# Performance work log

Hardware: AMD Instinct MI355X
Metric: run time of the kernel (lower is better)

Reference implementation:

```python
import jax, jax.numpy as jnp
import numpy as np
import math

B, N, SEEDS, DIM, H = 16, 2048, 4, 512, 8
DS = DIM // H
EPS = 1e-5
LOG_2PI = math.log(2.0 * math.pi)


def setup_inputs() -> dict:
    key = jax.random.key(0)
    ks = jax.random.split(key, 12)
    s = 1.0 / math.sqrt(DIM)
    d = {}
    d["X"] = jax.random.normal(ks[0], (B, N, SEEDS, DIM), jnp.float32)
    # seed parameters (kaiming/xavier-ish init)
    d["M"] = jax.random.uniform(ks[1], (1, SEEDS, DIM), jnp.float32, -s, s) * math.sqrt(6.0)
    d["S"] = jax.random.uniform(ks[2], (1, SEEDS, DIM), jnp.float32, -s, s) * math.sqrt(6.0)
    d["p"] = jax.random.uniform(ks[3], (1, SEEDS), jnp.float32, -0.5, 0.5)
    # linear layers (PyTorch Linear: y = x @ W.T + b)
    d["Wk"] = jax.random.uniform(ks[4], (DIM, DIM), jnp.float32, -s, s)
    d["bk"] = jax.random.uniform(ks[5], (DIM,), jnp.float32, -s, s)
    d["Wv"] = jax.random.uniform(ks[6], (DIM, DIM), jnp.float32, -s, s)
    d["bv"] = jax.random.uniform(ks[7], (DIM,), jnp.float32, -s, s)
    d["Wo"] = jax.random.uniform(ks[8], (DIM, DIM), jnp.float32, -s, s)
    d["bo"] = jax.random.uniform(ks[9], (DIM,), jnp.float32, -s, s)
    # batchnorm affine params (init: weight=1, bias=0)
    d["g0"] = jnp.ones((SEEDS * DIM,), jnp.float32)
    d["b0"] = jnp.zeros((SEEDS * DIM,), jnp.float32)
    d["g1"] = jnp.ones((SEEDS * DIM,), jnp.float32)
    d["b1"] = jnp.zeros((SEEDS * DIM,), jnp.float32)
    return d


def _batchnorm(x, g, b):
    # BatchNorm1d in training mode: batch stats (biased variance), eps=1e-5
    m = x.mean(axis=0)
    v = x.var(axis=0)
    return g * (x - m) / jnp.sqrt(v + EPS) + b


def reference(X, M, S, p, Wk, bk, Wv, bv, Wo, bo, g0, b0, g1, b1):
    mu = M[0].reshape(SEEDS, H, DS)                      # [S,H,DS] per-head seeds
    sigma = jax.nn.softplus(S[0]).reshape(SEEDS, H, DS)  # [S,H,DS]
    logp = jnp.log(jax.nn.softmax(p[0], axis=-1))        # [S]

    K = (X @ Wk.T + bk).reshape(B, N, SEEDS, H, DS)
    V = (X @ Wv.T + bv).reshape(B, N, SEEDS, H, DS)

    # GMM log-likelihood scores: sum over per-head feature dim
    diff = K - mu                                        # [B,N,S,H,DS]
    ll = (-0.5 * LOG_2PI - jnp.log(sigma) - 0.5 * diff * diff / (sigma * sigma)).sum(-1)
    ll = ll + logp[:, None]                              # [B,N,S,H]

    A = jax.nn.softmax(ll / math.sqrt(DIM), axis=1)      # softmax over instances n
    O = mu + jnp.einsum('bnsh,bnshd->bshd', A, V)        # [B,S,H,DS]
    O = O.reshape(B, SEEDS, DIM)                         # head-major feature concat

    O = _batchnorm(O.reshape(B, SEEDS * DIM), g0, b0).reshape(B, SEEDS, DIM)
    O = O + jax.nn.relu(O @ Wo.T + bo)
    O = _batchnorm(O.reshape(B, SEEDS * DIM), g1, b1).reshape(B, SEEDS, DIM)
    return O
```

## Files before the change

### kernel.cpp

```cpp
#include <hip/hip_runtime.h>
#include <hip/hip_bf16.h>

typedef __attribute__((ext_vector_type(4))) float f32x4;
typedef __attribute__((ext_vector_type(8))) short bf16x8;

constexpr int NB = 16, NN = 2048, NS = 4, NDIM = 512, NH = 8, NDS = 64;
constexpr float LOG2PI = 1.8378770664093453f;
constexpr float INV_SQRT_DIM = 0.04419417382415922f;

__device__ inline short f2bf(float f) {
  __hip_bfloat16 h = __float2bfloat16(f);
  return *reinterpret_cast<short*>(&h);
}
__device__ inline float bf2f(short b) {
  union { unsigned u; float f; } v;
  v.u = ((unsigned)(unsigned short)b) << 16;
  return v.f;
}

__device__ inline void gld16(const void* g, void* l) {
  __builtin_amdgcn_global_load_lds(
      (const __attribute__((address_space(1))) void*)g,
      (__attribute__((address_space(3))) void*)l, 16, 0, 0);
}

__global__ __launch_bounds__(256) void prepcvt_kernel(
    const float* __restrict__ Wv, float* __restrict__ WvT,
    const float* __restrict__ Wk, short* __restrict__ Wkb,
    const float* __restrict__ Mp, const float* __restrict__ Sp,
    const float* __restrict__ pp, const float* __restrict__ bkp,
    float4* __restrict__ gmm, float* __restrict__ lp2,
    const float* __restrict__ X, short* __restrict__ Xb)
{
  const int blk = blockIdx.x;
  const int tid = threadIdx.x;
  if (blk < 1024) {
    const int idx = blk * 256 + tid;
    const int d = idx & 63;
    const int i = (idx >> 6) & 511;
    const int h = idx >> 15;
    WvT[idx] = Wv[(size_t)(h * 64 + d) * 512 + i];
  } else if (blk < 1152) {
    const int j = (blk - 1024) * 256 + tid;
    const float4 a = reinterpret_cast<const float4*>(Wk)[(size_t)j * 2];
    const float4 b = reinterpret_cast<const float4*>(Wk)[(size_t)j * 2 + 1];
    bf16x8 o;
    o[0] = f2bf(a.x); o[1] = f2bf(a.y); o[2] = f2bf(a.z); o[3] = f2bf(a.w);
    o[4] = f2bf(b.x); o[5] = f2bf(b.y); o[6] = f2bf(b.z); o[7] = f2bf(b.w);
    *reinterpret_cast<bf16x8*>(&Wkb[(size_t)j * 8]) = o;
  } else if (blk < 1160) {
    const int idx = (blk - 1152) * 256 + tid;
    const int Jg = idx & 511;
    const float sv = Sp[idx];
    const float sig = log1pf(expf(sv));
    float4 o;
    o.x = Mp[idx];
    o.y = (-0.5f * LOG2PI - logf(sig)) * INV_SQRT_DIM;
    o.z = (0.5f / (sig * sig)) * INV_SQRT_DIM;
    o.w = bkp[Jg];
    gmm[idx] = o;
    if (idx < 4) {
      const float p0 = pp[0], p1 = pp[1], p2 = pp[2], p3 = pp[3];
      const float pmx = fmaxf(fmaxf(p0, p1), fmaxf(p2, p3));
      const float lse = pmx + logf(expf(p0 - pmx) + expf(p1 - pmx) +
                                   expf(p2 - pmx) + expf(p3 - pmx));
      lp2[idx] = (pp[idx] - lse) * INV_SQRT_DIM;
    }
  } else {
    const int stride = 2048 * 256;
    for (int i = (blk - 1160) * 256 + tid; i < 8388608; i += stride) {
      const float4 a = reinterpret_cast<const float4*>(X)[(size_t)i * 2];
      const float4 b = reinterpret_cast<const float4*>(X)[(size_t)i * 2 + 1];
      bf16x8 o;
      o[0] = f2bf(a.x); o[1] = f2bf(a.y); o[2] = f2bf(a.z); o[3] = f2bf(a.w);
      o[4] = f2bf(b.x); o[5] = f2bf(b.y); o[6] = f2bf(b.z); o[7] = f2bf(b.w);
      *reinterpret_cast<bf16x8*>(&Xb[(size_t)i * 8]) = o;
    }
  }
}

__global__ __launch_bounds__(256) void kproj_kernel(
    const short* __restrict__ Xb, const short* __restrict__ Wkb,
    const float4* __restrict__ gmm, const float* __restrict__ lp2,
    float* __restrict__ ll_ws)
{
  __shared__ short As[2][128 * 64];
  __shared__ short Bs[2][128 * 64];

  const int bid0 = blockIdx.x;
  const int bid = (bid0 & 7) * 512 + (bid0 >> 3);
  const int ct = bid & 3;
  const int mt = bid >> 2;
  const int m0 = mt * 128;
  const int c0 = ct * 128;

  const int t = threadIdx.x;
  const int l = t & 63;
  const int w = t >> 6;
  const int wr = w >> 1, wc = w & 1;
  const int lg = l >> 4, lr = l & 15;

  f32x4 acc[4][4] = {};

  const int g8 = (l & 7) ^ (l >> 3);
  const size_t gxa = (size_t)(m0 + w * 32 + (l >> 3)) * NDIM + g8 * 8;
  const size_t gba = (size_t)(c0 + w * 32 + (l >> 3)) * NDIM + g8 * 8;
  const int dA = (w * 32) * 64;

  auto stage = [&](int buf, int ts) {
    const int k0 = ts << 6;
    #pragma unroll
    for (int q = 0; q < 4; ++q) {
      const size_t so = (size_t)(q * 8) * NDIM + k0;
      const int dd = dA + (q * 8) * 64;
      gld16(&Xb[gxa + so],  (char*)&As[buf][dd]);
      gld16(&Wkb[gba + so], (char*)&Bs[buf][dd]);
    }
  };

  auto compute = [&](int buf) {
    #pragma unroll
    for (int kk = 0; kk < 64; kk += 32) {
      bf16x8 a[4], b[4];
      #pragma unroll
      for (int i = 0; i < 4; ++i) {
        const int r = wr * 64 + i * 16 + lr;
        const int byte = r * 128 + ((((kk >> 3) + lg) ^ (lr & 7)) << 4);
        a[i] = *reinterpret_cast<const bf16x8*>((const char*)&As[buf][0] + byte);
      }
      #pragma unroll
      for (int j = 0; j < 4; ++j) {
        const int r = wc * 64 + j * 16 + lr;
        const int byte = r * 128 + ((((kk >> 3) + lg) ^ (lr & 7)) << 4);
        b[j] = *reinterpret_cast<const bf16x8*>((const char*)&Bs[buf][0] + byte);
      }
      #pragma unroll
      for (int i = 0; i < 4; ++i) {
        #pragma unroll
        for (int j = 0; j < 4; ++j)
          acc[i][j] = __builtin_amdgcn_mfma_f32_16x16x32_bf16(a[i], b[j], acc[i][j], 0, 0, 0);
      }
    }
  };

  stage(0, 0);
  __builtin_amdgcn_sched_barrier(0);
  for (int ts = 0; ts < 7; ++ts) {
    stage((ts + 1) & 1, ts + 1);
    asm volatile("s_waitcnt vmcnt(8)" ::: "memory");
    __builtin_amdgcn_s_barrier();
    compute(ts & 1);
    __builtin_amdgcn_s_barrier();
  }
  asm volatile("s_waitcnt vmcnt(0)" ::: "memory");
  __builtin_amdgcn_s_barrier();
  compute(1);
  __builtin_amdgcn_sched_barrier(0);


  const float l0 = lp2[0], l1 = lp2[1], l2 = lp2[2], l3 = lp2[3];
  const float lpv[4] = {l0, l1, l2, l3};

  float part[4][4];
  #pragma unroll
  for (int i = 0; i < 4; ++i)
    #pragma unroll
    for (int e = 0; e < 4; ++e) part[i][e] = 0.f;

  #pragma unroll
  for (int j = 0; j < 4; ++j) {
    const int Jg = c0 + wc * 64 + j * 16 + lr;
    #pragma unroll
    for (int e = 0; e < 4; ++e) {
      const float4 gw = gmm[e * NDIM + Jg];
      #pragma unroll
      for (int i = 0; i < 4; ++i) {
        const float kv = acc[i][j][e] + gw.w;
        const float d = kv - gw.x;
        part[i][e] += gw.y - d * d * gw.z;
      }
    }
  }
  #pragma unroll
  for (int off = 1; off < 16; off <<= 1) {
    #pragma unroll
    for (int i = 0; i < 4; ++i)
      #pragma unroll
      for (int e = 0; e < 4; ++e)
        part[i][e] += __shfl_xor(part[i][e], off, 64);
  }
  if (lr == 0) {
    const int h = ct * 2 + wc;
    #pragma unroll
    for (int i = 0; i < 4; ++i) {
      #pragma unroll
      for (int e = 0; e < 4; ++e) {
        const int R = m0 + wr * 64 + i * 16 + 4 * lg + e;
        const int bn = R >> 2;
        const int bb = bn >> 11;
        const int nn = bn & (NN - 1);
        ll_ws[((size_t)((bb * NS + e) * NH + h)) * NN + nn] = part[i][e] + lpv[e];
      }
    }
  }
}

__global__ __launch_bounds__(256) void y_kernel(
    const float* __restrict__ ll_ws, const short* __restrict__ Xb,
    float* __restrict__ Yp, float2* __restrict__ msws)
{
  __shared__ float wT[256][8];
  __shared__ float redm[8][4];
  __shared__ float reds[8][4];
  const int blk = blockIdx.x;
  const int bs = blk & 63;
  const int nq = blk >> 6;
  const int b = bs >> 2, s = bs & 3;
  const int g0 = bs * 8;
  const int t = threadIdx.x;
  const int w = t >> 6, l = t & 63;

  float lv[8];
  #pragma unroll
  for (int h = 0; h < 8; ++h) {
    lv[h] = ll_ws[(size_t)(g0 + h) * NN + nq * 256 + t];
    float mm = lv[h];
    #pragma unroll
    for (int off = 1; off < 64; off <<= 1) mm = fmaxf(mm, __shfl_xor(mm, off, 64));
    if (l == 0) redm[h][w] = mm;
  }
  __syncthreads();
  float mx[8];
  #pragma unroll
  for (int h = 0; h < 8; ++h) {
    mx[h] = fmaxf(fmaxf(redm[h][0], redm[h][1]), fmaxf(redm[h][2], redm[h][3]));
    const float e = expf(lv[h] - mx[h]);
    wT[t][h] = e;
    float ss = e;
    #pragma unroll
    for (int off = 1; off < 64; off <<= 1) ss += __shfl_xor(ss, off, 64);
    if (l == 0) reds[h][w] = ss;
  }
  __syncthreads();
  if (t < 8) {
    const float sum = reds[t][0] + reds[t][1] + reds[t][2] + reds[t][3];
    msws[(size_t)(g0 + t) * 8 + nq] = make_float2(mx[t], sum);
  }

  const ushort2* X2 = reinterpret_cast<const ushort2*>(Xb);
  const size_t xbase = ((size_t)(b * 2048 + nq * 256) * 4 + s) * 256 + t;
  float acc[8][2] = {};
  #pragma unroll 4
  for (int n = 0; n < 256; ++n) {
    const ushort2 xv = X2[xbase + (size_t)n * 1024];
    const float x0 = bf2f((short)xv.x), x1 = bf2f((short)xv.y);
    const float4 w0 = *reinterpret_cast<const float4*>(&wT[n][0]);
    const float4 w1 = *reinterpret_cast<const float4*>(&wT[n][4]);
    acc[0][0] += w0.x * x0; acc[0][1] += w0.x * x1;
    acc[1][0] += w0.y * x0; acc[1][1] += w0.y * x1;
    acc[2][0] += w0.z * x0; acc[2][1] += w0.z * x1;
    acc[3][0] += w0.w * x0; acc[3][1] += w0.w * x1;
    acc[4][0] += w1.x * x0; acc[4][1] += w1.x * x1;
    acc[5][0] += w1.y * x0; acc[5][1] += w1.y * x1;
    acc[6][0] += w1.z * x0; acc[6][1] += w1.z * x1;
    acc[7][0] += w1.w * x0; acc[7][1] += w1.w * x1;
  }
  #pragma unroll
  for (int h = 0; h < 8; ++h) {
    float* yp = Yp + ((size_t)((nq * 64 + bs) * 8 + h)) * 512 + 2 * t;
    yp[0] = acc[h][0]; yp[1] = acc[h][1];
  }
}

__global__ __launch_bounds__(256) void poolproj_kernel(
    const float* __restrict__ Yp, const float2* __restrict__ msws,
    const float* __restrict__ WvT, const float* __restrict__ bvp,
    const float* __restrict__ Mp, float* __restrict__ O0)
{
  __shared__ float ys[512];
  __shared__ float pr[4][64];
  const int g = blockIdx.x;
  const int bs = g >> 3, h = g & 7;
  const int s = bs & 3;
  const int t = threadIdx.x;

  const float2* msp = msws + (size_t)g * 8;
  float M = -1e30f;
  #pragma unroll
  for (int q = 0; q < 8; ++q) M = fmaxf(M, msp[q].x);
  float cq[8];
  float S = 0.f;
  #pragma unroll
  for (int q = 0; q < 8; ++q) {
    cq[q] = expf(msp[q].x - M);
    S += msp[q].y * cq[q];
  }
  const float rS = 1.f / S;

  float a0 = 0.f, a1 = 0.f;
  #pragma unroll
  for (int q = 0; q < 8; ++q) {
    const float* yp = Yp + ((size_t)((q * 64 + bs) * 8 + h)) * 512;
    const float c = cq[q] * rS;
    a0 += yp[t] * c;
    a1 += yp[t + 256] * c;
  }
  ys[t] = a0; ys[t + 256] = a1;
  __syncthreads();

  const int d = t & 63, p = t >> 6;
  const float* wt = WvT + ((size_t)h * 512 + p * 128) * 64 + d;
  const float* yy = ys + p * 128;
  float acc = 0.f;
  #pragma unroll 4
  for (int i = 0; i < 128; ++i) acc += yy[i] * wt[(size_t)i * 64];
  pr[p][d] = acc;
  __syncthreads();
  if (t < 64) {
    const float tot = pr[0][t] + pr[1][t] + pr[2][t] + pr[3][t];
    O0[(size_t)g * 64 + t] = Mp[s * NDIM + h * NDS + t] + bvp[h * 64 + t] + tot;
  }
}

__global__ __launch_bounds__(256) void bnmlp_kernel(
    const float* __restrict__ O0, const float* __restrict__ gg,
    const float* __restrict__ bb, const float* __restrict__ Wo,
    const float* __restrict__ bo, float* __restrict__ Zo)
{
  __shared__ float ys[512];
  const int blk = blockIdx.x;
  const int t = threadIdx.x;
  const int r = blk >> 1;
  const int b = r >> 2, s = r & 3;

  #pragma unroll
  for (int u = 0; u < 2; ++u) {
    const int i = u * 256 + t;
    const int f = s * 512 + i;
    float x[NB];
    float m = 0.f;
    #pragma unroll
    for (int bq = 0; bq < NB; ++bq) { x[bq] = O0[bq * 2048 + f]; m += x[bq]; }
    m *= (1.f / NB);
    float v = 0.f;
    #pragma unroll
    for (int bq = 0; bq < NB; ++bq) { const float d = x[bq] - m; v += d * d; }
    v *= (1.f / NB);
    const float inv = rsqrtf(v + 1e-5f) * gg[f];
    ys[i] = (x[b] - m) * inv + bb[f];
  }
  __syncthreads();

  const int j = ((blk & 1) << 8) + t;
  const float4* yv = reinterpret_cast<const float4*>(ys);
  const float4* wrow = reinterpret_cast<const float4*>(Wo + (size_t)j * NDIM);
  float acc = 0.f;
  #pragma unroll 4
  for (int i = 0; i < 128; ++i) {
    const float4 a = yv[i], w = wrow[i];
    acc += a.x * w.x + a.y * w.y + a.z * w.z + a.w * w.w;
  }
  Zo[(size_t)r * 512 + j] = ys[j] + fmaxf(acc + bo[j], 0.f);
}

__global__ __launch_bounds__(256) void bn_kernel(
    const float* __restrict__ Xin, const float* __restrict__ gg,
    const float* __restrict__ bb, float* __restrict__ Yo)
{
  const int f = blockIdx.x * 256 + threadIdx.x;
  float x[NB];
  float m = 0.f;
  #pragma unroll
  for (int b = 0; b < NB; ++b) { x[b] = Xin[b * (NS * NDIM) + f]; m += x[b]; }
  m *= (1.f / NB);
  float v = 0.f;
  #pragma unroll
  for (int b = 0; b < NB; ++b) { const float d = x[b] - m; v += d * d; }
  v *= (1.f / NB);
  const float inv = rsqrtf(v + 1e-5f) * gg[f];
  const float bf = bb[f];
  #pragma unroll
  for (int b = 0; b < NB; ++b) Yo[b * (NS * NDIM) + f] = (x[b] - m) * inv + bf;
}

extern "C" void kernel_launch(void* const* d_in, const int* in_sizes, int n_in,
                              void* d_out, int out_size, void* d_ws, size_t ws_size,
                              hipStream_t stream) {
  (void)in_sizes; (void)n_in; (void)out_size; (void)ws_size;
  const float* X  = (const float*)d_in[0];
  const float* M  = (const float*)d_in[1];
  const float* S  = (const float*)d_in[2];
  const float* p  = (const float*)d_in[3];
  const float* Wk = (const float*)d_in[4];
  const float* bk = (const float*)d_in[5];
  const float* Wv = (const float*)d_in[6];
  const float* bv = (const float*)d_in[7];
  const float* Wo = (const float*)d_in[8];
  const float* bo = (const float*)d_in[9];
  const float* g0 = (const float*)d_in[10];
  const float* b0 = (const float*)d_in[11];
  const float* g1 = (const float*)d_in[12];
  const float* b1 = (const float*)d_in[13];

  char* ws = (char*)d_ws;
  short* Xb    = (short*)ws;
  float* ll_ws = (float*)(ws + (size_t)134217728);
  float* Yp    = (float*)(ws + (size_t)138416128);
  float* O0    = (float*)(ws + (size_t)146804736);
  float* Z     = (float*)(ws + (size_t)147066880);
  short* Wkb   = (short*)(ws + (size_t)147197952);
  float* WvT   = (float*)(ws + (size_t)147722240);
  float4* gmm  = (float4*)(ws + (size_t)148770816);
  float* lp2   = (float*)(ws + (size_t)148803584);
  float2* msws = (float2*)(ws + (size_t)148803712);

  prepcvt_kernel<<<3208, 256, 0, stream>>>(Wv, WvT, Wk, Wkb, M, S, p, bk,
                                           gmm, lp2, X, Xb);
  kproj_kernel<<<4096, 256, 0, stream>>>(Xb, Wkb, gmm, lp2, ll_ws);
  y_kernel<<<512, 256, 0, stream>>>(ll_ws, Xb, Yp, msws);
  poolproj_kernel<<<512, 256, 0, stream>>>(Yp, msws, WvT, bv, M, O0);
  bnmlp_kernel<<<128, 256, 0, stream>>>(O0, g0, b0, Wo, bo, Z);
  bn_kernel<<<8, 256, 0, stream>>>(Z, g1, b1, (float*)d_out);
}
```

Baseline: 255.8 us.

## Fuse X fp32-to-bf16 conversion into first K-projection column tile

The standalone pass that converted all of X to bf16 is removed. A new kproj1 kernel handles column tile 0: it loads fp32 X through registers, converts it to bf16, writes it to both LDS and the global Xb buffer, and computes its GEMM tile. A second kernel, kproj2, runs the remaining three column tiles from the bf16 Xb. This removes one full read of the fp32 X tensor and one kernel's worth of traffic, at the cost of a register-staged A path in kproj1 and an extra launch.

```diff
diff --git a/kernel.cpp b/kernel.cpp
--- a/kernel.cpp
+++ b/kernel.cpp
@@ -24,13 +24,12 @@
       (__attribute__((address_space(3))) void*)l, 16, 0, 0);
 }
 
-__global__ __launch_bounds__(256) void prepcvt_kernel(
+__global__ __launch_bounds__(256) void prep_kernel(
     const float* __restrict__ Wv, float* __restrict__ WvT,
     const float* __restrict__ Wk, short* __restrict__ Wkb,
     const float* __restrict__ Mp, const float* __restrict__ Sp,
     const float* __restrict__ pp, const float* __restrict__ bkp,
-    float4* __restrict__ gmm, float* __restrict__ lp2,
-    const float* __restrict__ X, short* __restrict__ Xb)
+    float4* __restrict__ gmm, float* __restrict__ lp2)
 {
   const int blk = blockIdx.x;
   const int tid = threadIdx.x;
@@ -48,7 +47,7 @@
     o[0] = f2bf(a.x); o[1] = f2bf(a.y); o[2] = f2bf(a.z); o[3] = f2bf(a.w);
     o[4] = f2bf(b.x); o[5] = f2bf(b.y); o[6] = f2bf(b.z); o[7] = f2bf(b.w);
     *reinterpret_cast<bf16x8*>(&Wkb[(size_t)j * 8]) = o;
-  } else if (blk < 1160) {
+  } else {
     const int idx = (blk - 1152) * 256 + tid;
     const int Jg = idx & 511;
     const float sv = Sp[idx];
@@ -66,33 +65,21 @@
                                    expf(p2 - pmx) + expf(p3 - pmx));
       lp2[idx] = (pp[idx] - lse) * INV_SQRT_DIM;
     }
-  } else {
-    const int stride = 2048 * 256;
-    for (int i = (blk - 1160) * 256 + tid; i < 8388608; i += stride) {
-      const float4 a = reinterpret_cast<const float4*>(X)[(size_t)i * 2];
-      const float4 b = reinterpret_cast<const float4*>(X)[(size_t)i * 2 + 1];
-      bf16x8 o;
-      o[0] = f2bf(a.x); o[1] = f2bf(a.y); o[2] = f2bf(a.z); o[3] = f2bf(a.w);
-      o[4] = f2bf(b.x); o[5] = f2bf(b.y); o[6] = f2bf(b.z); o[7] = f2bf(b.w);
-      *reinterpret_cast<bf16x8*>(&Xb[(size_t)i * 8]) = o;
-    }
-  }
-}
-
-__global__ __launch_bounds__(256) void kproj_kernel(
-    const short* __restrict__ Xb, const short* __restrict__ Wkb,
+  }
+}
+
+__global__ __launch_bounds__(256) void kproj1_kernel(
+    const float* __restrict__ X, const short* __restrict__ Wkb,
     const float4* __restrict__ gmm, const float* __restrict__ lp2,
-    float* __restrict__ ll_ws)
+    float* __restrict__ ll_ws, short* __restrict__ Xb)
 {
   __shared__ short As[2][128 * 64];
   __shared__ short Bs[2][128 * 64];
 
   const int bid0 = blockIdx.x;
-  const int bid = (bid0 & 7) * 512 + (bid0 >> 3);
-  const int ct = bid & 3;
-  const int mt = bid >> 2;
+  const int mt = (bid0 & 7) * 128 + (bid0 >> 3);
   const int m0 = mt * 128;
-  const int c0 = ct * 128;
+  const int c0 = 0;
 
   const int t = threadIdx.x;
   const int l = t & 63;
@@ -103,6 +90,163 @@
   f32x4 acc[4][4] = {};
 
   const int g8 = (l & 7) ^ (l >> 3);
+  const size_t gba = (size_t)(c0 + w * 32 + (l >> 3)) * NDIM + g8 * 8;
+  const int dB = (w * 32) * 64;
+  auto stageB = [&](int buf, int ts) {
+    const int k0 = ts << 6;
+    #pragma unroll
+    for (int q = 0; q < 4; ++q)
+      gld16(&Wkb[gba + (size_t)(q * 8) * NDIM + k0], (char*)&Bs[buf][dB + q * 8 * 64]);
+  };
+
+  float4 rA[4][2];
+  auto issueA = [&](int ts) {
+    const int k0 = ts << 6;
+    #pragma unroll
+    for (int u = 0; u < 4; ++u) {
+      const int bc = u * 256 + t;
+      const int row = bc >> 3, c = bc & 7;
+      const float* src = &X[(size_t)(m0 + row) * NDIM + k0 + c * 8];
+      rA[u][0] = *reinterpret_cast<const float4*>(src);
+      rA[u][1] = *reinterpret_cast<const float4*>(src + 4);
+    }
+  };
+  auto cvtWriteA = [&](int buf, int ts) {
+    const int k0 = ts << 6;
+    #pragma unroll
+    for (int u = 0; u < 4; ++u) {
+      const int bc = u * 256 + t;
+      const int row = bc >> 3, c = bc & 7;
+      bf16x8 o;
+      o[0] = f2bf(rA[u][0].x); o[1] = f2bf(rA[u][0].y);
+      o[2] = f2bf(rA[u][0].z); o[3] = f2bf(rA[u][0].w);
+      o[4] = f2bf(rA[u][1].x); o[5] = f2bf(rA[u][1].y);
+      o[6] = f2bf(rA[u][1].z); o[7] = f2bf(rA[u][1].w);
+      *reinterpret_cast<bf16x8*>(
+          (char*)&As[buf][0] + row * 128 + ((c ^ (row & 7)) << 4)) = o;
+      *reinterpret_cast<bf16x8*>(&Xb[(size_t)(m0 + row) * NDIM + k0 + c * 8]) = o;
+    }
+  };
+
+  auto compute = [&](int buf) {
+    #pragma unroll
+    for (int kk = 0; kk < 64; kk += 32) {
+      bf16x8 a[4], b[4];
+      #pragma unroll
+      for (int i = 0; i < 4; ++i) {
+        const int r = wr * 64 + i * 16 + lr;
+        const int byte = r * 128 + ((((kk >> 3) + lg) ^ (lr & 7)) << 4);
+        a[i] = *reinterpret_cast<const bf16x8*>((const char*)&As[buf][0] + byte);
+      }
+      #pragma unroll
+      for (int j = 0; j < 4; ++j) {
+        const int r = wc * 64 + j * 16 + lr;
+        const int byte = r * 128 + ((((kk >> 3) + lg) ^ (lr & 7)) << 4);
+        b[j] = *reinterpret_cast<const bf16x8*>((const char*)&Bs[buf][0] + byte);
+      }
+      #pragma unroll
+      for (int i = 0; i < 4; ++i) {
+        #pragma unroll
+        for (int j = 0; j < 4; ++j)
+          acc[i][j] = __builtin_amdgcn_mfma_f32_16x16x32_bf16(a[i], b[j], acc[i][j], 0, 0, 0);
+      }
+    }
+  };
+
+  issueA(0);
+  cvtWriteA(0, 0);
+  stageB(0, 0);
+  issueA(1);
+  asm volatile("s_waitcnt vmcnt(8)" ::: "memory");
+  asm volatile("s_waitcnt lgkmcnt(0)" ::: "memory");
+  __builtin_amdgcn_s_barrier();
+  __builtin_amdgcn_sched_barrier(0);
+  for (int ts = 0; ts < 7; ++ts) {
+    cvtWriteA((ts + 1) & 1, ts + 1);
+    stageB((ts + 1) & 1, ts + 1);
+    if (ts < 6) issueA(ts + 2);
+    asm volatile("s_waitcnt lgkmcnt(0)" ::: "memory");
+    __builtin_amdgcn_s_barrier();
+    compute(ts & 1);
+    __builtin_amdgcn_s_barrier();
+  }
+  asm volatile("s_waitcnt vmcnt(0)" ::: "memory");
+  __builtin_amdgcn_s_barrier();
+  compute(1);
+  __builtin_amdgcn_sched_barrier(0);
+
+  const float l0 = lp2[0], l1 = lp2[1], l2 = lp2[2], l3 = lp2[3];
+  const float lpv[4] = {l0, l1, l2, l3};
+
+  float part[4][4];
+  #pragma unroll
+  for (int i = 0; i < 4; ++i)
+    #pragma unroll
+    for (int e = 0; e < 4; ++e) part[i][e] = 0.f;
+
+  #pragma unroll
+  for (int j = 0; j < 4; ++j) {
+    const int Jg = c0 + wc * 64 + j * 16 + lr;
+    #pragma unroll
+    for (int e = 0; e < 4; ++e) {
+      const float4 gw = gmm[e * NDIM + Jg];
+      #pragma unroll
+      for (int i = 0; i < 4; ++i) {
+        const float kv = acc[i][j][e] + gw.w;
+        const float d = kv - gw.x;
+        part[i][e] += gw.y - d * d * gw.z;
+      }
+    }
+  }
+  #pragma unroll
+  for (int off = 1; off < 16; off <<= 1) {
+    #pragma unroll
+    for (int i = 0; i < 4; ++i)
+      #pragma unroll
+      for (int e = 0; e < 4; ++e)
+        part[i][e] += __shfl_xor(part[i][e], off, 64);
+  }
+  if (lr == 0) {
+    const int h = wc;
+    #pragma unroll
+    for (int i = 0; i < 4; ++i) {
+      #pragma unroll
+      for (int e = 0; e < 4; ++e) {
+        const int R = m0 + wr * 64 + i * 16 + 4 * lg + e;
+        const int bn = R >> 2;
+        const int bb = bn >> 11;
+        const int nn = bn & (NN - 1);
+        ll_ws[((size_t)((bb * NS + e) * NH + h)) * NN + nn] = part[i][e] + lpv[e];
+      }
+    }
+  }
+}
+
+__global__ __launch_bounds__(256) void kproj2_kernel(
+    const short* __restrict__ Xb, const short* __restrict__ Wkb,
+    const float4* __restrict__ gmm, const float* __restrict__ lp2,
+    float* __restrict__ ll_ws)
+{
+  __shared__ short As[2][128 * 64];
+  __shared__ short Bs[2][128 * 64];
+
+  const int bid0 = blockIdx.x;
+  const int xcd = bid0 & 7;
+  const int q = bid0 >> 3;
+  const int mt = xcd * 128 + q / 3;
+  const int ct = 1 + q % 3;
+  const int m0 = mt * 128;
+  const int c0 = ct * 128;
+
+  const int t = threadIdx.x;
+  const int l = t & 63;
+  const int w = t >> 6;
+  const int wr = w >> 1, wc = w & 1;
+  const int lg = l >> 4, lr = l & 15;
+
+  f32x4 acc[4][4] = {};
+
+  const int g8 = (l & 7) ^ (l >> 3);
   const size_t gxa = (size_t)(m0 + w * 32 + (l >> 3)) * NDIM + g8 * 8;
   const size_t gba = (size_t)(c0 + w * 32 + (l >> 3)) * NDIM + g8 * 8;
   const int dA = (w * 32) * 64;
@@ -110,9 +254,9 @@
   auto stage = [&](int buf, int ts) {
     const int k0 = ts << 6;
     #pragma unroll
-    for (int q = 0; q < 4; ++q) {
-      const size_t so = (size_t)(q * 8) * NDIM + k0;
-      const int dd = dA + (q * 8) * 64;
+    for (int qq = 0; qq < 4; ++qq) {
+      const size_t so = (size_t)(qq * 8) * NDIM + k0;
+      const int dd = dA + (qq * 8) * 64;
       gld16(&Xb[gxa + so],  (char*)&As[buf][dd]);
       gld16(&Wkb[gba + so], (char*)&Bs[buf][dd]);
     }
@@ -156,7 +300,6 @@
   __builtin_amdgcn_s_barrier();
   compute(1);
   __builtin_amdgcn_sched_barrier(0);
-
 
   const float l0 = lp2[0], l1 = lp2[1], l2 = lp2[2], l3 = lp2[3];
   const float lpv[4] = {l0, l1, l2, l3};
@@ -414,9 +557,9 @@
   float* lp2   = (float*)(ws + (size_t)148803584);
   float2* msws = (float2*)(ws + (size_t)148803712);
 
-  prepcvt_kernel<<<3208, 256, 0, stream>>>(Wv, WvT, Wk, Wkb, M, S, p, bk,
-                                           gmm, lp2, X, Xb);
-  kproj_kernel<<<4096, 256, 0, stream>>>(Xb, Wkb, gmm, lp2, ll_ws);
+  prep_kernel<<<1160, 256, 0, stream>>>(Wv, WvT, Wk, Wkb, M, S, p, bk, gmm, lp2);
+  kproj1_kernel<<<1024, 256, 0, stream>>>(X, Wkb, gmm, lp2, ll_ws, Xb);
+  kproj2_kernel<<<3072, 256, 0, stream>>>(Xb, Wkb, gmm, lp2, ll_ws);
   y_kernel<<<512, 256, 0, stream>>>(ll_ws, Xb, Yp, msws);
   poolproj_kernel<<<512, 256, 0, stream>>>(Yp, msws, WvT, bv, M, O0);
   bnmlp_kernel<<<128, 256, 0, stream>>>(O0, g0, b0, Wo, bo, Z);
```

Result: faster. 236.3 us, median of 2 (-7.6%).
